# Kernel optimization log

Hardware: AMD Instinct MI355X
Metric: run time of the kernel (lower is better)

Reference implementation:

```python
import jax, jax.numpy as jnp
import numpy as np

CLIP_VALUE = 5.0  # matches init clip_value


def setup_inputs() -> dict:
    B, T, I, H = 256, 400, 256, 512
    key = jax.random.key(0)
    k_x, k_ih, k_hh = jax.random.split(key, 3)
    scale = 1.0 / np.sqrt(I + H)  # is_encoder=True -> scale_dim = input+hidden
    x = jax.random.normal(k_x, (B, T, I), dtype=jnp.float32)
    h0 = jnp.zeros((B, H), dtype=jnp.float32)
    weight_ih = jax.random.normal(k_ih, (3 * H, I), dtype=jnp.float32) * scale
    weight_hh = jax.random.normal(k_hh, (3 * H, H), dtype=jnp.float32) * scale
    # bias_ih: ones, with the last H entries (new-gate bias) zeroed
    bias_ih = jnp.concatenate([jnp.ones(2 * H, jnp.float32), jnp.zeros(H, jnp.float32)])
    bias_hh = jnp.zeros(3 * H, dtype=jnp.float32)  # frozen zeros in the original
    return {"x": x, "h0": h0, "weight_ih": weight_ih, "bias_ih": bias_ih,
            "weight_hh": weight_hh, "bias_hh": bias_hh}


def reference(x, h0, weight_ih, bias_ih, weight_hh, bias_hh):
    H = h0.shape[-1]
    W_zr = weight_hh[:2 * H]          # [2H, H]
    W_n = weight_hh[2 * H:]           # [H, H]
    b_zr = bias_hh[:2 * H]
    b_n = bias_hh[2 * H:]
    # Precompute all input projections in one big GEMM: [B, T, 3H]
    x_all = jnp.einsum('bti,gi->btg', x, weight_ih) + bias_ih
    x_all_t = jnp.transpose(x_all, (1, 0, 2))  # time-major [T, B, 3H]

    def step(h, x_t):
        x_z, x_r, x_n = jnp.split(x_t, 3, axis=-1)
        h_zr = h @ W_zr.T + b_zr
        h_z, h_r = jnp.split(h_zr, 2, axis=-1)
        z = jax.nn.sigmoid(x_z + h_z)
        r = jax.nn.sigmoid(x_r + h_r)
        # NOTE: faithful to source precedence: (r * hidden) @ W_n^T + b_n
        h_n = (r * h) @ W_n.T + b_n
        n = jnp.tanh(x_n + h_n)
        h_new = z * h + (1.0 - z) * n
        h_new = jnp.clip(h_new, -CLIP_VALUE, CLIP_VALUE)
        return h_new, h_new

    h_last, out_t = jax.lax.scan(step, h0, x_all_t)
    output = jnp.transpose(out_t, (1, 0, 2))  # [B, T, H]
    return output, h_last
```

## Files before the change

### kernel.cpp

```cpp
#include <hip/hip_runtime.h>
#include <stdint.h>

#define B_DIM 256
#define T_DIM 400
#define I_DIMM 256
#define H_DIM 512
#define KH 512
#define KX 256
#define KU 768
#define MT 32
#define ACOLS 32
#define BCOLS 16
#define LDK 776

#define LDS_USHORTS (2*ACOLS*LDK + 2*BCOLS*LDK)
#define LDS_BYTES   (LDS_USHORTS*2 + (512 + 1280)*4)

#define OFF_FLAGA 0
#define OFF_FLAGB 1024
#define OFF_HFRAG 8192
#define FRAG_BYTES (16*16*64*32)
#define OFF_RHFRAG (OFF_HFRAG + FRAG_BYTES)
#define OFF_ZBUF   (OFF_RHFRAG + FRAG_BYTES)
#define OFF_XFRAG  (OFF_ZBUF + B_DIM*H_DIM*4)
#define XFRAG_BYTES ((size_t)T_DIM*16*8*2048)
#define WS_NEED    ((size_t)OFF_XFRAG + XFRAG_BYTES)

typedef unsigned long long u64;
typedef __attribute__((ext_vector_type(8))) short short8v;
typedef __attribute__((ext_vector_type(4))) float f32x4;
typedef __attribute__((ext_vector_type(4))) unsigned uint4v;
typedef __attribute__((ext_vector_type(2))) u64 u64x2;

__device__ __forceinline__ unsigned short f2bf(float f){
  unsigned u = __builtin_bit_cast(unsigned, f);
  return (unsigned short)((u + 0x7fffu + ((u >> 16) & 1u)) >> 16);
}
__device__ __forceinline__ float bf2f(unsigned short u){
  return __builtin_bit_cast(float, ((unsigned)u) << 16);
}
__device__ __forceinline__ f32x4 mfma16(short8v a, short8v b, f32x4 c){
  return __builtin_amdgcn_mfma_f32_16x16x32_bf16(a, b, c, 0, 0, 0);
}

__device__ __forceinline__ u64 ld64_cg(const void* p){
  return __hip_atomic_load((const u64*)p, __ATOMIC_RELAXED, __HIP_MEMORY_SCOPE_AGENT);
}
__device__ __forceinline__ unsigned ld16_cg(const void* p){
  return (unsigned)__hip_atomic_load((const unsigned short*)p, __ATOMIC_RELAXED,
                                     __HIP_MEMORY_SCOPE_AGENT);
}
__device__ __forceinline__ void cst128(void* p, uint4v v){
  asm volatile("global_store_dwordx4 %0, %1, off sc0 sc1" :: "v"(p), "v"(v) : "memory");
}
#define VMCNT0() asm volatile("s_waitcnt vmcnt(0)" ::: "memory")

__device__ __forceinline__ void spin32(const unsigned* f, unsigned target){
  const u64* p = (const u64*)(f + ((threadIdx.x & 15) << 1));
  for (;;){
    u64 v = __hip_atomic_load(p, __ATOMIC_RELAXED, __HIP_MEMORY_SCOPE_AGENT);
    bool ok = ((unsigned)v >= target) & ((unsigned)(v >> 32) >= target);
    if (__all((int)ok)) break;
    __builtin_amdgcn_s_sleep(1);
  }
  asm volatile("" ::: "memory");
}

__device__ __forceinline__ size_t frag_off(int row, int col){
  int fragblk = (row >> 5)*2 + ((row >> 4) & 1);
  int kb   = col >> 5;
  int lane = (row & 15) + (((col & 31) >> 3) << 4);
  int e    = col & 7;
  return (size_t)fragblk*32768 + kb*2048 + lane*32 + e*2;
}

__global__ void gru_init(const float* __restrict__ h0, char* __restrict__ ws){
  int gtid = blockIdx.x * blockDim.x + threadIdx.x;
  if (gtid < 2048) ((unsigned*)ws)[gtid] = 0u;
  char* hfrag = ws + OFF_HFRAG;
  for (int idx = gtid; idx < B_DIM*H_DIM; idx += gridDim.x * blockDim.x){
    float h = h0[idx];
    unsigned short hi = f2bf(h);
    unsigned short lo = f2bf(h - bf2f(hi));
    size_t off = frag_off(idx >> 9, idx & 511);
    *(unsigned short*)(hfrag + off)      = hi;
    *(unsigned short*)(hfrag + off + 16) = lo;
  }
}

__global__ void x_transcode(const float* __restrict__ x, char* __restrict__ xfrag){
  int gtid = blockIdx.x * blockDim.x + threadIdx.x;
  int w = gtid >> 6, lane = gtid & 63;
  if (w >= T_DIM*16*8) return;
  int t = w >> 7, rem = w & 127, rb = rem >> 3, kb = rem & 7;
  int row = rb*16 + (lane & 15);
  int kq  = (lane >> 4) * 8;
  const float* src = x + ((size_t)row*T_DIM + t)*I_DIMM + kb*32 + kq;
  f32x4 v0 = *(const f32x4*)src;
  f32x4 v1 = *(const f32x4*)(src + 4);
  short8v hi, lo;
  #pragma unroll
  for (int e = 0; e < 4; ++e){
    unsigned short h0b = f2bf(v0[e]), h1b = f2bf(v1[e]);
    hi[e] = (short)h0b;  hi[e+4] = (short)h1b;
    lo[e]   = (short)f2bf(v0[e] - bf2f(h0b));
    lo[e+4] = (short)f2bf(v1[e] - bf2f(h1b));
  }
  char* dst = xfrag + ((size_t)(t*16 + rb)*8 + kb)*2048 + lane*32;
  *(short8v*)dst = hi;
  *(short8v*)(dst + 16) = lo;
}

template<int XF>
__global__ void __launch_bounds__(256, 1) gru_scan(
    const float* __restrict__ x, const float* __restrict__ w_ih,
    const float* __restrict__ b_ih, const float* __restrict__ w_hh,
    const float* __restrict__ b_hh, const float* __restrict__ h0,
    float* __restrict__ out, char* __restrict__ ws)
{
  extern __shared__ unsigned short lds[];
  unsigned short* WAh = lds;
  unsigned short* WAl = WAh + ACOLS*LDK;
  unsigned short* WBh = WAl + ACOLS*LDK;
  unsigned short* WBl = WBh + BCOLS*LDK;
  float* red   = (float*)(WBl + BCOLS*LDK);
  float* tpose = red + 512;

  char* hfrag  = ws + OFF_HFRAG;
  char* rhfrag = ws + OFF_RHFRAG;
  float* zbuf  = (float*)(ws + OFF_ZBUF);
  const char* xfrag = ws + OFF_XFRAG;

  const int bid = blockIdx.x;
  const int it  = bid & 7;
  const int j   = bid >> 3;
  const int tid = threadIdx.x;
  const int lane = tid & 63;
  const int wv   = tid >> 6;
  unsigned* flagsA = (unsigned*)(ws + OFF_FLAGA) + it*32;
  unsigned* flagsB = (unsigned*)(ws + OFF_FLAGB) + it*32;

  for (int c = 0; c < ACOLS; ++c){
    int g = ACOLS*j + c;
    for (int k = tid; k < KU; k += 256){
      float w = (k < KH) ? w_hh[(size_t)g*KH + k] : w_ih[(size_t)g*KX + (k - KH)];
      unsigned short hi = f2bf(w);
      WAh[c*LDK + k] = hi;
      WAl[c*LDK + k] = f2bf(w - bf2f(hi));
    }
  }
  for (int c = 0; c < BCOLS; ++c){
    int g = 1024 + BCOLS*j + c;
    for (int k = tid; k < KU; k += 256){
      float w = (k < KH) ? w_hh[(size_t)g*KH + k] : w_ih[(size_t)g*KX + (k - KH)];
      unsigned short hi = f2bf(w);
      WBh[c*LDK + k] = hi;
      WBl[c*LDK + k] = f2bf(w - bf2f(hi));
    }
  }
  __syncthreads();

  const int l16 = lane & 15;
  const int lq  = lane >> 4;
  const int kq  = lq * 8;
  const int rowblk  = wv & 1;
  const int colblkA = wv >> 1;
  const int khalf   = wv >> 1;

  const int fragblk = it*2 + rowblk;
  const char* hA_base  = hfrag  + (size_t)fragblk*32768 + lane*32;
  const char* rhB_base = rhfrag + (size_t)fragblk*32768 + lane*32;
  const int arow = it*MT + rowblk*16 + l16;
  const size_t xrow_off = (size_t)arow * (T_DIM*I_DIMM);
  const int ldsA = (colblkA*16 + l16) * LDK;
  const int ldsB = l16 * LDK;

  const int zr = ACOLS*j + colblkA*16 + l16;
  const float biasA = b_ih[zr] + b_hh[zr];
  const int nc = BCOLS*j + l16;
  const float biasB = b_ih[1024 + nc] + b_hh[1024 + nc];
  const int mrow0 = it*MT + rowblk*16 + lq*4;

  const int hcs = zr & 511;
  size_t off_hv[4];
  #pragma unroll
  for (int r = 0; r < 4; ++r) off_hv[r] = frag_off(mrow0 + r, hcs);

  float* zst = zbuf + ((size_t)it*512 + hcs)*32 + rowblk*16 + lq*4;
  const float* zld = zbuf + ((size_t)it*512 + nc)*32 + rowblk*16 + lq*4;
  char* rhkb = rhfrag + (size_t)fragblk*32768 + (size_t)((j - 16) & 15)*2048;
  char* hkb  = hfrag  + (size_t)fragblk*32768 + (size_t)(j >> 1)*2048;

  u64 hb0[4][4], hb1[4][4];

  auto LDH = [&](u64 (&buf)[4][4], int c0){
    #pragma unroll
    for (int u = 0; u < 4; ++u){
      const char* p = hA_base + (size_t)(c0*4 + u)*2048;
      buf[u][0] = ld64_cg(p);      buf[u][1] = ld64_cg(p + 8);
      buf[u][2] = ld64_cg(p + 16); buf[u][3] = ld64_cg(p + 24);
    }
  };
  auto PRA = [&](u64 (&buf)[4][4], int c0, f32x4& D){
    #pragma unroll
    for (int u = 0; u < 4; ++u){
      int k0 = (c0*4 + u)*32 + kq;
      u64x2 thi = {buf[u][0], buf[u][1]};
      u64x2 tlo = {buf[u][2], buf[u][3]};
      short8v ah = __builtin_bit_cast(short8v, thi);
      short8v al = __builtin_bit_cast(short8v, tlo);
      short8v bh = *(const short8v*)(WAh + ldsA + k0);
      short8v bl = *(const short8v*)(WAl + ldsA + k0);
      D = mfma16(ah, bh, D); D = mfma16(ah, bl, D); D = mfma16(al, bh, D);
    }
  };
  auto LDR = [&](u64 (&buf)[4][4], int c0){
    #pragma unroll
    for (int u = 0; u < 4; ++u){
      const char* p = rhB_base + (size_t)((khalf*8) + c0*4 + u)*2048;
      buf[u][0] = ld64_cg(p);      buf[u][1] = ld64_cg(p + 8);
      buf[u][2] = ld64_cg(p + 16); buf[u][3] = ld64_cg(p + 24);
    }
  };
  auto PRB = [&](u64 (&buf)[4][4], int c0, f32x4& D){
    #pragma unroll
    for (int u = 0; u < 4; ++u){
      int k0 = ((khalf*8) + c0*4 + u)*32 + kq;
      u64x2 thi = {buf[u][0], buf[u][1]};
      u64x2 tlo = {buf[u][2], buf[u][3]};
      short8v ah = __builtin_bit_cast(short8v, thi);
      short8v al = __builtin_bit_cast(short8v, tlo);
      short8v bh = *(const short8v*)(WBh + ldsB + k0);
      short8v bl = *(const short8v*)(WBl + ldsB + k0);
      D = mfma16(ah, bh, D); D = mfma16(ah, bl, D); D = mfma16(al, bh, D);
    }
  };
  auto XCONV = [&](const float* xp, short8v& ah, short8v& al){
    f32x4 v0 = *(const f32x4*)xp;
    f32x4 v1 = *(const f32x4*)(xp + 4);
    #pragma unroll
    for (int e = 0; e < 4; ++e){
      unsigned short h0b = f2bf(v0[e]), h1b = f2bf(v1[e]);
      ah[e] = (short)h0b;  ah[e+4] = (short)h1b;
      al[e]   = (short)f2bf(v0[e] - bf2f(h0b));
      al[e+4] = (short)f2bf(v1[e] - bf2f(h1b));
    }
  };
  auto TPOSE = [&](const float (&v)[4], char* fragkb, int colq_base){
    float* tw = tpose + wv*320;
    #pragma unroll
    for (int r = 0; r < 4; ++r) tw[(lq*4 + r)*20 + l16] = v[r];
    int b = (lane >> 4) & 1;
    const float* tr = tpose + wv*320 + (lane & 15)*20 + b*8;
    f32x4 w0 = *(const f32x4*)tr;
    f32x4 w1 = *(const f32x4*)(tr + 4);
    uint4v wd;
    if (lane < 32){
      unsigned h0b=f2bf(w0[0]), h1b=f2bf(w0[1]), h2b=f2bf(w0[2]), h3b=f2bf(w0[3]);
      unsigned h4b=f2bf(w1[0]), h5b=f2bf(w1[1]), h6b=f2bf(w1[2]), h7b=f2bf(w1[3]);
      wd.x = h0b | (h1b<<16); wd.y = h2b | (h3b<<16);
      wd.z = h4b | (h5b<<16); wd.w = h6b | (h7b<<16);
    } else {
      unsigned l0=f2bf(w0[0]-bf2f(f2bf(w0[0]))), l1=f2bf(w0[1]-bf2f(f2bf(w0[1])));
      unsigned l2=f2bf(w0[2]-bf2f(f2bf(w0[2]))), l3=f2bf(w0[3]-bf2f(f2bf(w0[3])));
      unsigned l4=f2bf(w1[0]-bf2f(f2bf(w1[0]))), l5=f2bf(w1[1]-bf2f(f2bf(w1[1])));
      unsigned l6=f2bf(w1[2]-bf2f(f2bf(w1[2]))), l7=f2bf(w1[3]-bf2f(f2bf(w1[3])));
      wd.x = l0 | (l1<<16); wd.y = l2 | (l3<<16);
      wd.z = l4 | (l5<<16); wd.w = l6 | (l7<<16);
    }
    int fl = (lane & 15) + (colq_base + b)*16;
    cst128(fragkb + fl*32 + ((lane < 32) ? 0 : 16), wd);
  };

  float h_reg[4];
  if (khalf == 0){
    #pragma unroll
    for (int r = 0; r < 4; ++r)
      h_reg[r] = h0[(size_t)(mrow0 + r)*H_DIM + nc];
  }

  for (int t = 0; t < T_DIM; ++t){
    const char* xf_base = xfrag + ((size_t)t*16 + fragblk)*8*2048 + lane*32;
    const float* xt = x + (size_t)t * I_DIMM;

    f32x4 D = {0.f, 0.f, 0.f, 0.f};
    #pragma unroll
    for (int kb = 0; kb < 8; ++kb){
      short8v ah, al;
      if (XF){
        const char* p = xf_base + kb*2048;
        ah = *(const short8v*)p;
        al = *(const short8v*)(p + 16);
      } else {
        XCONV(xt + xrow_off + kb*32 + kq, ah, al);
      }
      int k0 = KH + kb*32 + kq;
      short8v bh = *(const short8v*)(WAh + ldsA + k0);
      short8v bl = *(const short8v*)(WAl + ldsA + k0);
      D = mfma16(ah, bh, D); D = mfma16(ah, bl, D); D = mfma16(al, bh, D);
    }

    spin32(flagsB, (unsigned)t);

    unsigned hvh[4], hvl[4];
    #pragma unroll
    for (int r = 0; r < 4; ++r){
      hvh[r] = ld16_cg(hfrag + off_hv[r]);
      hvl[r] = ld16_cg(hfrag + off_hv[r] + 16);
    }
    LDH(hb0, 0); LDH(hb1, 1);
    PRA(hb0, 0, D); LDH(hb0, 2);
    PRA(hb1, 1, D); LDH(hb1, 3);
    PRA(hb0, 2, D); PRA(hb1, 3, D);

    if (j < 16){
      f32x4 zq;
      #pragma unroll
      for (int r = 0; r < 4; ++r){
        float a = D[r] + biasA;
        zq[r] = 1.f / (1.f + __expf(-a));
      }
      cst128(zst, __builtin_bit_cast(uint4v, zq));
    } else {
      float rhv[4];
      #pragma unroll
      for (int r = 0; r < 4; ++r){
        float a = D[r] + biasA;
        float rv = 1.f / (1.f + __expf(-a));
        rhv[r] = rv * (bf2f((unsigned short)hvh[r]) + bf2f((unsigned short)hvl[r]));
      }
      TPOSE(rhv, rhkb, colblkA*2);
    }
    VMCNT0();
    __syncthreads();
    if (tid == 0)
      __hip_atomic_store(flagsA + j, (unsigned)(t+1), __ATOMIC_RELAXED,
                         __HIP_MEMORY_SCOPE_AGENT);

    f32x4 Dn = {0.f, 0.f, 0.f, 0.f};
    #pragma unroll
    for (int u = 0; u < 4; ++u){
      int kb = khalf*4 + u;
      short8v ah, al;
      if (XF){
        const char* p = xf_base + kb*2048;
        ah = *(const short8v*)p;
        al = *(const short8v*)(p + 16);
      } else {
        XCONV(xt + xrow_off + kb*32 + kq, ah, al);
      }
      int k0 = KH + kb*32 + kq;
      short8v bh = *(const short8v*)(WBh + ldsB + k0);
      short8v bl = *(const short8v*)(WBl + ldsB + k0);
      Dn = mfma16(ah, bh, Dn); Dn = mfma16(ah, bl, Dn); Dn = mfma16(al, bh, Dn);
    }

    spin32(flagsA, (unsigned)(t+1));

    f32x4 zq = {0.f, 0.f, 0.f, 0.f};
    if (khalf == 0){
      u64 z0 = ld64_cg(zld), z1 = ld64_cg((const char*)zld + 8);
      u64x2 zz = {z0, z1};
      zq = __builtin_bit_cast(f32x4, zz);
    }
    LDR(hb0, 0); LDR(hb1, 1);
    PRB(hb0, 0, Dn);
    PRB(hb1, 1, Dn);

    if (khalf == 1){
      #pragma unroll
      for (int r = 0; r < 4; ++r)
        red[rowblk*256 + (lq*4 + r)*16 + l16] = Dn[r];
    }
    __syncthreads();
    float hn[4];
    if (khalf == 0){
      #pragma unroll
      for (int r = 0; r < 4; ++r){
        float a = Dn[r] + red[rowblk*256 + (lq*4 + r)*16 + l16] + biasB;
        float ea = __expf(2.f * fabsf(a));
        float nv = 1.f - 2.f / (ea + 1.f);
        nv = (a < 0.f) ? -nv : nv;
        float hnv = zq[r]*h_reg[r] + (1.f - zq[r])*nv;
        hnv = fminf(5.f, fmaxf(-5.f, hnv));
        hn[r] = hnv;
        h_reg[r] = hnv;
      }
      TPOSE(hn, hkb, (j & 1)*2);
    }
    VMCNT0();
    __syncthreads();
    if (tid == 0)
      __hip_atomic_store(flagsB + j, (unsigned)(t+1), __ATOMIC_RELAXED,
                         __HIP_MEMORY_SCOPE_AGENT);
    if (khalf == 0){
      #pragma unroll
      for (int r = 0; r < 4; ++r){
        int row = mrow0 + r;
        out[(size_t)row*(T_DIM*H_DIM) + (size_t)t*H_DIM + nc] = hn[r];
        if (t == T_DIM - 1)
          out[(size_t)B_DIM*T_DIM*H_DIM + (size_t)row*H_DIM + nc] = hn[r];
      }
    }
  }
}

extern "C" void kernel_launch(void* const* d_in, const int* in_sizes, int n_in,
                              void* d_out, int out_size, void* d_ws, size_t ws_size,
                              hipStream_t stream){
  const float* x    = (const float*)d_in[0];
  const float* h0   = (const float*)d_in[1];
  const float* w_ih = (const float*)d_in[2];
  const float* b_ih = (const float*)d_in[3];
  const float* w_hh = (const float*)d_in[4];
  const float* b_hh = (const float*)d_in[5];
  float* out = (float*)d_out;
  char* ws = (char*)d_ws;

  gru_init<<<128, 256, 0, stream>>>(h0, ws);

  if (ws_size >= WS_NEED){
    x_transcode<<<(T_DIM*16*8*64 + 255)/256, 256, 0, stream>>>(x, ws + OFF_XFRAG);
    hipFuncSetAttribute((const void*)gru_scan<1>,
                        hipFuncAttributeMaxDynamicSharedMemorySize, LDS_BYTES);
    gru_scan<1><<<256, 256, LDS_BYTES, stream>>>(x, w_ih, b_ih, w_hh, b_hh, h0, out, ws);
  } else {
    hipFuncSetAttribute((const void*)gru_scan<0>,
                        hipFuncAttributeMaxDynamicSharedMemorySize, LDS_BYTES);
    gru_scan<0><<<256, 256, LDS_BYTES, stream>>>(x, w_ih, b_ih, w_hh, b_hh, h0, out, ws);
  }
}
```

Before: 5.194 ms.

## Split z/r gate GEMM across K halves with LDS reduction and rotated load order

The z/r phase changes from each wave pair owning a 16-column block over the full K to each wave computing both 16-column blocks over half of K. The halves are then summed through an LDS reduction, matching how the n-gate phase already works. The start of the K-block load order is rotated per workgroup so that many blocks do not hit the same hfrag/rhfrag chunks at once, and the LDS row pitch is shrunk. This halves the serial MFMA chain per wave on the critical recurrent path, at the cost of an extra __syncthreads and LDS round trip per step.

New measurement: 4.894 ms. -5.8%, faster.

```diff
diff --git a/kernel.cpp b/kernel.cpp
--- a/kernel.cpp
+++ b/kernel.cpp
@@ -11,10 +11,10 @@
 #define MT 32
 #define ACOLS 32
 #define BCOLS 16
-#define LDK 776
+#define LDK 772
 
 #define LDS_USHORTS (2*ACOLS*LDK + 2*BCOLS*LDK)
-#define LDS_BYTES   (LDS_USHORTS*2 + (512 + 1280)*4)
+#define LDS_BYTES   (LDS_USHORTS*2 + (1024 + 640)*4)
 
 #define OFF_FLAGA 0
 #define OFF_FLAGB 1024
@@ -124,7 +124,7 @@
   unsigned short* WBh = WAl + ACOLS*LDK;
   unsigned short* WBl = WBh + BCOLS*LDK;
   float* red   = (float*)(WBl + BCOLS*LDK);
-  float* tpose = red + 512;
+  float* tpose = red + 1024;
 
   char* hfrag  = ws + OFF_HFRAG;
   char* rhfrag = ws + OFF_RHFRAG;
@@ -163,69 +163,79 @@
   const int l16 = lane & 15;
   const int lq  = lane >> 4;
   const int kq  = lq * 8;
-  const int rowblk  = wv & 1;
-  const int colblkA = wv >> 1;
-  const int khalf   = wv >> 1;
+  const int rowblk = wv & 1;
+  const int khalf  = wv >> 1;
 
   const int fragblk = it*2 + rowblk;
   const char* hA_base  = hfrag  + (size_t)fragblk*32768 + lane*32;
   const char* rhB_base = rhfrag + (size_t)fragblk*32768 + lane*32;
   const int arow = it*MT + rowblk*16 + l16;
   const size_t xrow_off = (size_t)arow * (T_DIM*I_DIMM);
-  const int ldsA = (colblkA*16 + l16) * LDK;
-  const int ldsB = l16 * LDK;
-
-  const int zr = ACOLS*j + colblkA*16 + l16;
-  const float biasA = b_ih[zr] + b_hh[zr];
+  const int ldsA0 = l16 * LDK;
+  const int ldsA1 = (16 + l16) * LDK;
+  const int ldsB  = l16 * LDK;
+
+  const int zr0 = ACOLS*j + l16;
+  const int zr1 = zr0 + 16;
+  const float biasA0 = b_ih[zr0] + b_hh[zr0];
+  const float biasA1 = b_ih[zr1] + b_hh[zr1];
   const int nc = BCOLS*j + l16;
   const float biasB = b_ih[1024 + nc] + b_hh[1024 + nc];
   const int mrow0 = it*MT + rowblk*16 + lq*4;
 
-  const int hcs = zr & 511;
-  size_t off_hv[4];
+  const int hcs0 = zr0 & 511;
+  const int hcs1 = zr1 & 511;
+  size_t off_hv0[4], off_hv1[4];
   #pragma unroll
-  for (int r = 0; r < 4; ++r) off_hv[r] = frag_off(mrow0 + r, hcs);
-
-  float* zst = zbuf + ((size_t)it*512 + hcs)*32 + rowblk*16 + lq*4;
+  for (int r = 0; r < 4; ++r){
+    off_hv0[r] = frag_off(mrow0 + r, hcs0);
+    off_hv1[r] = frag_off(mrow0 + r, hcs1);
+  }
+
+  float* zst0 = zbuf + ((size_t)it*512 + hcs0)*32 + rowblk*16 + lq*4;
+  float* zst1 = zbuf + ((size_t)it*512 + hcs1)*32 + rowblk*16 + lq*4;
   const float* zld = zbuf + ((size_t)it*512 + nc)*32 + rowblk*16 + lq*4;
   char* rhkb = rhfrag + (size_t)fragblk*32768 + (size_t)((j - 16) & 15)*2048;
   char* hkb  = hfrag  + (size_t)fragblk*32768 + (size_t)(j >> 1)*2048;
 
-  u64 hb0[4][4], hb1[4][4];
-
-  auto LDH = [&](u64 (&buf)[4][4], int c0){
-    #pragma unroll
-    for (int u = 0; u < 4; ++u){
-      const char* p = hA_base + (size_t)(c0*4 + u)*2048;
+  u64 hb0[2][4], hb1[2][4];
+
+  auto LDH2 = [&](u64 (&buf)[2][4], int cc){
+    #pragma unroll
+    for (int u = 0; u < 2; ++u){
+      const char* p = hA_base + (size_t)(khalf*8 + cc*2 + u)*2048;
       buf[u][0] = ld64_cg(p);      buf[u][1] = ld64_cg(p + 8);
       buf[u][2] = ld64_cg(p + 16); buf[u][3] = ld64_cg(p + 24);
     }
   };
-  auto PRA = [&](u64 (&buf)[4][4], int c0, f32x4& D){
-    #pragma unroll
-    for (int u = 0; u < 4; ++u){
-      int k0 = (c0*4 + u)*32 + kq;
+  auto PRA2 = [&](u64 (&buf)[2][4], int cc, f32x4& D0, f32x4& D1){
+    #pragma unroll
+    for (int u = 0; u < 2; ++u){
+      int k0 = (khalf*8 + cc*2 + u)*32 + kq;
       u64x2 thi = {buf[u][0], buf[u][1]};
       u64x2 tlo = {buf[u][2], buf[u][3]};
       short8v ah = __builtin_bit_cast(short8v, thi);
       short8v al = __builtin_bit_cast(short8v, tlo);
-      short8v bh = *(const short8v*)(WAh + ldsA + k0);
-      short8v bl = *(const short8v*)(WAl + ldsA + k0);
-      D = mfma16(ah, bh, D); D = mfma16(ah, bl, D); D = mfma16(al, bh, D);
-    }
-  };
-  auto LDR = [&](u64 (&buf)[4][4], int c0){
-    #pragma unroll
-    for (int u = 0; u < 4; ++u){
-      const char* p = rhB_base + (size_t)((khalf*8) + c0*4 + u)*2048;
+      short8v bh0 = *(const short8v*)(WAh + ldsA0 + k0);
+      short8v bl0 = *(const short8v*)(WAl + ldsA0 + k0);
+      D0 = mfma16(ah, bh0, D0); D0 = mfma16(ah, bl0, D0); D0 = mfma16(al, bh0, D0);
+      short8v bh1 = *(const short8v*)(WAh + ldsA1 + k0);
+      short8v bl1 = *(const short8v*)(WAl + ldsA1 + k0);
+      D1 = mfma16(ah, bh1, D1); D1 = mfma16(ah, bl1, D1); D1 = mfma16(al, bh1, D1);
+    }
+  };
+  auto LDR2 = [&](u64 (&buf)[2][4], int cc){
+    #pragma unroll
+    for (int u = 0; u < 2; ++u){
+      const char* p = rhB_base + (size_t)(khalf*8 + cc*2 + u)*2048;
       buf[u][0] = ld64_cg(p);      buf[u][1] = ld64_cg(p + 8);
       buf[u][2] = ld64_cg(p + 16); buf[u][3] = ld64_cg(p + 24);
     }
   };
-  auto PRB = [&](u64 (&buf)[4][4], int c0, f32x4& D){
-    #pragma unroll
-    for (int u = 0; u < 4; ++u){
-      int k0 = ((khalf*8) + c0*4 + u)*32 + kq;
+  auto PRB2 = [&](u64 (&buf)[2][4], int cc, f32x4& D){
+    #pragma unroll
+    for (int u = 0; u < 2; ++u){
+      int k0 = (khalf*8 + cc*2 + u)*32 + kq;
       u64x2 thi = {buf[u][0], buf[u][1]};
       u64x2 tlo = {buf[u][2], buf[u][3]};
       short8v ah = __builtin_bit_cast(short8v, thi);
@@ -279,65 +289,14 @@
       h_reg[r] = h0[(size_t)(mrow0 + r)*H_DIM + nc];
   }
 
+  const int rotA = j & 3;
+  const int rotB = (j >> 2) & 3;
+
   for (int t = 0; t < T_DIM; ++t){
     const char* xf_base = xfrag + ((size_t)t*16 + fragblk)*8*2048 + lane*32;
     const float* xt = x + (size_t)t * I_DIMM;
 
-    f32x4 D = {0.f, 0.f, 0.f, 0.f};
-    #pragma unroll
-    for (int kb = 0; kb < 8; ++kb){
-      short8v ah, al;
-      if (XF){
-        const char* p = xf_base + kb*2048;
-        ah = *(const short8v*)p;
-        al = *(const short8v*)(p + 16);
-      } else {
-        XCONV(xt + xrow_off + kb*32 + kq, ah, al);
-      }
-      int k0 = KH + kb*32 + kq;
-      short8v bh = *(const short8v*)(WAh + ldsA + k0);
-      short8v bl = *(const short8v*)(WAl + ldsA + k0);
-      D = mfma16(ah, bh, D); D = mfma16(ah, bl, D); D = mfma16(al, bh, D);
-    }
-
-    spin32(flagsB, (unsigned)t);
-
-    unsigned hvh[4], hvl[4];
-    #pragma unroll
-    for (int r = 0; r < 4; ++r){
-      hvh[r] = ld16_cg(hfrag + off_hv[r]);
-      hvl[r] = ld16_cg(hfrag + off_hv[r] + 16);
-    }
-    LDH(hb0, 0); LDH(hb1, 1);
-    PRA(hb0, 0, D); LDH(hb0, 2);
-    PRA(hb1, 1, D); LDH(hb1, 3);
-    PRA(hb0, 2, D); PRA(hb1, 3, D);
-
-    if (j < 16){
-      f32x4 zq;
-      #pragma unroll
-      for (int r = 0; r < 4; ++r){
-        float a = D[r] + biasA;
-        zq[r] = 1.f / (1.f + __expf(-a));
-      }
-      cst128(zst, __builtin_bit_cast(uint4v, zq));
-    } else {
-      float rhv[4];
-      #pragma unroll
-      for (int r = 0; r < 4; ++r){
-        float a = D[r] + biasA;
-        float rv = 1.f / (1.f + __expf(-a));
-        rhv[r] = rv * (bf2f((unsigned short)hvh[r]) + bf2f((unsigned short)hvl[r]));
-      }
-      TPOSE(rhv, rhkb, colblkA*2);
-    }
-    VMCNT0();
-    __syncthreads();
-    if (tid == 0)
-      __hip_atomic_store(flagsA + j, (unsigned)(t+1), __ATOMIC_RELAXED,
-                         __HIP_MEMORY_SCOPE_AGENT);
-
-    f32x4 Dn = {0.f, 0.f, 0.f, 0.f};
+    f32x4 D0 = {0.f,0.f,0.f,0.f}, D1 = {0.f,0.f,0.f,0.f};
     #pragma unroll
     for (int u = 0; u < 4; ++u){
       int kb = khalf*4 + u;
@@ -350,6 +309,87 @@
         XCONV(xt + xrow_off + kb*32 + kq, ah, al);
       }
       int k0 = KH + kb*32 + kq;
+      short8v bh0 = *(const short8v*)(WAh + ldsA0 + k0);
+      short8v bl0 = *(const short8v*)(WAl + ldsA0 + k0);
+      D0 = mfma16(ah, bh0, D0); D0 = mfma16(ah, bl0, D0); D0 = mfma16(al, bh0, D0);
+      short8v bh1 = *(const short8v*)(WAh + ldsA1 + k0);
+      short8v bl1 = *(const short8v*)(WAl + ldsA1 + k0);
+      D1 = mfma16(ah, bh1, D1); D1 = mfma16(ah, bl1, D1); D1 = mfma16(al, bh1, D1);
+    }
+
+    spin32(flagsB, (unsigned)t);
+
+    unsigned hv0h[4], hv0l[4], hv1h[4], hv1l[4];
+    if (khalf == 0){
+      #pragma unroll
+      for (int r = 0; r < 4; ++r){
+        hv0h[r] = ld16_cg(hfrag + off_hv0[r]);
+        hv0l[r] = ld16_cg(hfrag + off_hv0[r] + 16);
+        hv1h[r] = ld16_cg(hfrag + off_hv1[r]);
+        hv1l[r] = ld16_cg(hfrag + off_hv1[r] + 16);
+      }
+    }
+    LDH2(hb0, (rotA+0)&3); LDH2(hb1, (rotA+1)&3);
+    PRA2(hb0, (rotA+0)&3, D0, D1); LDH2(hb0, (rotA+2)&3);
+    PRA2(hb1, (rotA+1)&3, D0, D1); LDH2(hb1, (rotA+3)&3);
+    PRA2(hb0, (rotA+2)&3, D0, D1);
+    PRA2(hb1, (rotA+3)&3, D0, D1);
+
+    if (khalf == 1){
+      #pragma unroll
+      for (int r = 0; r < 4; ++r){
+        red[(rowblk*2 + 0)*256 + (lq*4 + r)*16 + l16] = D0[r];
+        red[(rowblk*2 + 1)*256 + (lq*4 + r)*16 + l16] = D1[r];
+      }
+    }
+    __syncthreads();
+    if (khalf == 0){
+      #pragma unroll
+      for (int r = 0; r < 4; ++r){
+        D0[r] += red[(rowblk*2 + 0)*256 + (lq*4 + r)*16 + l16];
+        D1[r] += red[(rowblk*2 + 1)*256 + (lq*4 + r)*16 + l16];
+      }
+      if (j < 16){
+        f32x4 zq0, zq1;
+        #pragma unroll
+        for (int r = 0; r < 4; ++r){
+          zq0[r] = 1.f / (1.f + __expf(-(D0[r] + biasA0)));
+          zq1[r] = 1.f / (1.f + __expf(-(D1[r] + biasA1)));
+        }
+        cst128(zst0, __builtin_bit_cast(uint4v, zq0));
+        cst128(zst1, __builtin_bit_cast(uint4v, zq1));
+      } else {
+        float rhv0[4], rhv1[4];
+        #pragma unroll
+        for (int r = 0; r < 4; ++r){
+          float rv0 = 1.f / (1.f + __expf(-(D0[r] + biasA0)));
+          float rv1 = 1.f / (1.f + __expf(-(D1[r] + biasA1)));
+          rhv0[r] = rv0 * (bf2f((unsigned short)hv0h[r]) + bf2f((unsigned short)hv0l[r]));
+          rhv1[r] = rv1 * (bf2f((unsigned short)hv1h[r]) + bf2f((unsigned short)hv1l[r]));
+        }
+        TPOSE(rhv0, rhkb, 0);
+        TPOSE(rhv1, rhkb, 2);
+      }
+      VMCNT0();
+    }
+    __syncthreads();
+    if (tid == 0)
+      __hip_atomic_store(flagsA + j, (unsigned)(t+1), __ATOMIC_RELAXED,
+                         __HIP_MEMORY_SCOPE_AGENT);
+
+    f32x4 Dn = {0.f, 0.f, 0.f, 0.f};
+    #pragma unroll
+    for (int u = 0; u < 4; ++u){
+      int kb = khalf*4 + u;
+      short8v ah, al;
+      if (XF){
+        const char* p = xf_base + kb*2048;
+        ah = *(const short8v*)p;
+        al = *(const short8v*)(p + 16);
+      } else {
+        XCONV(xt + xrow_off + kb*32 + kq, ah, al);
+      }
+      int k0 = KH + kb*32 + kq;
       short8v bh = *(const short8v*)(WBh + ldsB + k0);
       short8v bl = *(const short8v*)(WBl + ldsB + k0);
       Dn = mfma16(ah, bh, Dn); Dn = mfma16(ah, bl, Dn); Dn = mfma16(al, bh, Dn);
@@ -363,21 +403,23 @@
       u64x2 zz = {z0, z1};
       zq = __builtin_bit_cast(f32x4, zz);
     }
-    LDR(hb0, 0); LDR(hb1, 1);
-    PRB(hb0, 0, Dn);
-    PRB(hb1, 1, Dn);
+    LDR2(hb0, (rotB+0)&3); LDR2(hb1, (rotB+1)&3);
+    PRB2(hb0, (rotB+0)&3, Dn); LDR2(hb0, (rotB+2)&3);
+    PRB2(hb1, (rotB+1)&3, Dn); LDR2(hb1, (rotB+3)&3);
+    PRB2(hb0, (rotB+2)&3, Dn);
+    PRB2(hb1, (rotB+3)&3, Dn);
 
     if (khalf == 1){
       #pragma unroll
       for (int r = 0; r < 4; ++r)
-        red[rowblk*256 + (lq*4 + r)*16 + l16] = Dn[r];
+        red[rowblk*512 + (lq*4 + r)*16 + l16] = Dn[r];
     }
     __syncthreads();
     float hn[4];
     if (khalf == 0){
       #pragma unroll
       for (int r = 0; r < 4; ++r){
-        float a = Dn[r] + red[rowblk*256 + (lq*4 + r)*16 + l16] + biasB;
+        float a = Dn[r] + red[rowblk*512 + (lq*4 + r)*16 + l16] + biasB;
         float ea = __expf(2.f * fabsf(a));
         float nv = 1.f - 2.f / (ea + 1.f);
         nv = (a < 0.f) ? -nv : nv;
@@ -387,8 +429,8 @@
         h_reg[r] = hnv;
       }
       TPOSE(hn, hkb, (j & 1)*2);
-    }
-    VMCNT0();
+      VMCNT0();
+    }
     __syncthreads();
     if (tid == 0)
       __hip_atomic_store(flagsB + j, (unsigned)(t+1), __ATOMIC_RELAXED,
```
